# Kernel tuning notes

Hardware: AMD Instinct MI355X
Metric: run time of the kernel (lower is better)

## Reference

```python
import jax, jax.numpy as jnp
import numpy as np

N_NODES = 2000
NEG_SLOPE = 0.01  # torch nn.LeakyReLU default


def setup_inputs() -> dict:
    key = jax.random.key(0)
    ks = jax.random.split(key, 7)
    B, T, N, F, E = 4, 12, N_NODES, 64, 32000
    state = jax.random.normal(ks[0], (B, T, N, F), dtype=jnp.float32)
    feature = jax.random.normal(ks[1], (N, F), dtype=jnp.float32)
    W = jax.random.normal(ks[2], (F, 2 * F), dtype=jnp.float32) / np.sqrt(2 * F)
    b = jnp.zeros((F,), dtype=jnp.float32)
    src = jax.random.randint(ks[3], (E,), 0, N)
    dst = jax.random.randint(ks[4], (E,), 0, N)
    dist = jax.random.uniform(ks[5], (E, 1), dtype=jnp.float32)
    return {"state": state, "feature": feature, "W": W, "b": b,
            "src": src, "dst": dst, "dist": dist}


def reference(state, feature, W, b, src, dst, dist):
    # state: [B,T,N,F] -> node-major [N,B,T,F] (matches unsqueeze/transpose/squeeze)
    s = jnp.moveaxis(state, 2, 0)                       # [N,B,T,F]
    s_src = s[src]                                      # [E,B,T,F] gather
    s_dst = s[dst]                                      # [E,B,T,F]
    h = jnp.concatenate([s_src, s_dst], axis=-1)        # [E,B,T,2F]
    alpha = jnp.einsum('ebtk,fk->ebtf', h, W) + b       # linear 2F->F
    alpha = jnp.where(alpha >= 0, alpha, NEG_SLOPE * alpha)  # LeakyReLU
    alpha = alpha * dist[:, None, None, :]              # dist [E,1] broadcast
    # segment softmax over incoming edges per destination node
    n = s.shape[0]
    m = jax.ops.segment_max(alpha, dst, num_segments=n)        # [N,B,T,F]
    ex = jnp.exp(alpha - m[dst])
    denom = jax.ops.segment_sum(ex, dst, num_segments=n)       # [N,B,T,F]
    w = ex / denom[dst]                                         # [E,B,T,F]
    new_state = jax.ops.segment_sum(w * s_src, dst, num_segments=n)
    new_state = jax.nn.relu(new_state)                  # [N,B,T,F]
    return jnp.moveaxis(new_state, 0, 2)                # [B,T,N,F]
```

## Files before the change

kernel.cpp:

```cpp
#include <hip/hip_runtime.h>
#include <hip/hip_bf16.h>
#include <hip/hip_fp16.h>
#include <math.h>


#define F_DIM 64
#define LOG2E 1.442695040888963f
#define CPAD 128
#define RSTRIDE 128

typedef _Float16 f16x8 __attribute__((ext_vector_type(8)));
typedef float f32x4 __attribute__((ext_vector_type(4)));

__global__ __launch_bounds__(256) void gemm_hist(
    const float* __restrict__ state, const float* __restrict__ W,
    const float* __restrict__ bias,
    unsigned* __restrict__ PSh, __half* __restrict__ P2Bh,
    const int* __restrict__ dst, int* __restrict__ chunk_hist,
    int E, int N, int HB) {
    __shared__ int h[2048];
    int tid = threadIdx.x;
    if ((int)blockIdx.x < HB) {
        int c = blockIdx.x;
        for (int i = tid; i < N; i += 256) h[i] = 0;
        __syncthreads();
        int e = c * 256 + tid;
        if (e < E) atomicAdd(&h[dst[e]], 1);
        __syncthreads();
        for (int d = tid; d < N; d += 256)
            chunk_hist[d * CPAD + c] = h[d];
        return;
    }
    int gb = blockIdx.x - HB;
    int wv = tid >> 6, lane = tid & 63;
    int l15 = lane & 15, l4 = lane >> 4;

    f16x8 bf[8][2];
#pragma unroll
    for (int ct = 0; ct < 8; ++ct) {
        int j = ct * 16 + l15;
        const float* wp = (j < 64) ? (W + j * 128) : (W + (j - 64) * 128 + 64);
#pragma unroll
        for (int kh = 0; kh < 2; ++kh) {
            const float* p = wp + kh * 32 + l4 * 8;
            float4 w0 = *(const float4*)p;
            float4 w1 = *(const float4*)(p + 4);
            f16x8 hh;
            hh[0] = (_Float16)w0.x; hh[1] = (_Float16)w0.y;
            hh[2] = (_Float16)w0.z; hh[3] = (_Float16)w0.w;
            hh[4] = (_Float16)w1.x; hh[5] = (_Float16)w1.y;
            hh[6] = (_Float16)w1.z; hh[7] = (_Float16)w1.w;
            bf[ct][kh] = hh;
        }
    }
    float b0 = bias[l15], b1 = bias[16 + l15], b2 = bias[32 + l15], b3 = bias[48 + l15];

    int r = gb * 64 + wv * 16;

    const float* ap = state + (long)(r + l15) * 64 + l4 * 8;
    float4 a0 = *(const float4*)ap;
    float4 a1 = *(const float4*)(ap + 4);
    float4 a2 = *(const float4*)(ap + 32);
    float4 a3 = *(const float4*)(ap + 36);
    f16x8 af0, af1;
    af0[0] = (_Float16)a0.x; af0[1] = (_Float16)a0.y;
    af0[2] = (_Float16)a0.z; af0[3] = (_Float16)a0.w;
    af0[4] = (_Float16)a1.x; af0[5] = (_Float16)a1.y;
    af0[6] = (_Float16)a1.z; af0[7] = (_Float16)a1.w;
    af1[0] = (_Float16)a2.x; af1[1] = (_Float16)a2.y;
    af1[2] = (_Float16)a2.z; af1[3] = (_Float16)a2.w;
    af1[4] = (_Float16)a3.x; af1[5] = (_Float16)a3.y;
    af1[6] = (_Float16)a3.z; af1[7] = (_Float16)a3.w;

    f32x4 zero = {0.f, 0.f, 0.f, 0.f};
    f32x4 acc[8];
#pragma unroll
    for (int ct = 0; ct < 8; ++ct) {
        acc[ct] = __builtin_amdgcn_mfma_f32_16x16x32_f16(af0, bf[ct][0], zero, 0, 0, 0);
        acc[ct] = __builtin_amdgcn_mfma_f32_16x16x32_f16(af1, bf[ct][1], acc[ct], 0, 0, 0);
    }

    float bb0[4] = {b0, b1, b2, b3};
#pragma unroll
    for (int reg = 0; reg < 4; ++reg) {
        long rr = r + l4 * 4 + reg;
        const float* sp = state + rr * 64;
#pragma unroll
        for (int ct = 0; ct < 4; ++ct) {
            float sval = sp[ct * 16 + l15];
            __half2 hh = __floats2half2_rn(acc[ct][reg], sval);
            PSh[rr * 64 + ct * 16 + l15] = *(unsigned*)&hh;
        }
#pragma unroll
        for (int ct = 4; ct < 8; ++ct) {
            P2Bh[rr * 64 + (ct - 4) * 16 + l15] =
                __float2half(acc[ct][reg] + bb0[ct - 4]);
        }
    }
}

__global__ void binscan_kernel(int* __restrict__ chunk_hist, int* __restrict__ counts,
                               int* __restrict__ esrc, float* __restrict__ edist,
                               int N, int C) {
    int wave = (blockIdx.x * blockDim.x + threadIdx.x) >> 6;
    int lane = threadIdx.x & 63;
    if (wave >= N) return;
    int* row = chunk_hist + wave * CPAD;
    int i0 = 2 * lane, i1 = 2 * lane + 1;
    int v0 = (i0 < C) ? row[i0] : 0;
    int v1 = (i1 < C) ? row[i1] : 0;
    int s = v0 + v1;
    int acc = s;
#pragma unroll
    for (int d = 1; d < 64; d <<= 1) {
        int up = __shfl_up(acc, d);
        if (lane >= d) acc += up;
    }
    int excl = acc - s;
    if (i0 < C) row[i0] = excl;
    if (i1 < C) row[i1] = excl + v0;
    int total = __shfl(acc, 63);
    if (lane == 63) counts[wave] = total;
    int* er = esrc + wave * RSTRIDE;
    float* dr = edist + wave * RSTRIDE;
    if (i0 >= total) { er[i0] = 0; dr[i0] = 0.f; }
    if (i1 >= total) { er[i1] = 0; dr[i1] = 0.f; }
}

__global__ void scatter2_kernel(const int* __restrict__ dst, const int* __restrict__ src,
                                const float* __restrict__ dist,
                                const int* __restrict__ chunk_hist,
                                int* __restrict__ esrc, float* __restrict__ edist, int E) {
    __shared__ int sdst[256];
    int t = threadIdx.x, c = blockIdx.x;
    int e = c * 256 + t;
    int d = (e < E) ? dst[e] : -1;
    sdst[t] = d;
    __syncthreads();
    if (e >= E) return;
    int cnt = 0;
#pragma unroll 8
    for (int j = 0; j < 256; j++)
        cnt += (j < t && sdst[j] == d) ? 1 : 0;
    int off = chunk_hist[d * CPAD + c] + cnt;
    if (off < RSTRIDE) {
        esrc[d * RSTRIDE + off] = src[e] << 8;
        edist[d * RSTRIDE + off] = dist[e] * LOG2E;
    }
}


#define ECOMP(U, D, P2V, DEN, NUM)                                        \
    {                                                                     \
        float x;                                                          \
        asm("v_fma_mix_f32 %0, %1, %2, %3 op_sel:[0,0,0] op_sel_hi:[1,0,0]" \
            : "=v"(x) : "v"(U), "v"(fone), "v"(P2V));                     \
        float y0 = x * (D);                                               \
        float y1 = 0.01f * y0;                                            \
        float y = fmaxf(y0, y1);                                          \
        float p = __builtin_amdgcn_exp2f(y);                              \
        DEN += p;                                                         \
        asm("v_fma_mix_f32 %0, %1, %2, %0 op_sel:[0,1,0] op_sel_hi:[0,1,0]" \
            : "+v"(NUM) : "v"(p), "v"(U));                                \
    }

#define G4E4(EP, DP, Q, P2V, D0, D1, M0, M1)                              \
    {                                                                     \
        int4   sq = (EP)[Q];                                              \
        float4 dq = (DP)[Q];                                              \
        unsigned q0 = *(const unsigned*)(PSb + sq.x + f4);                \
        unsigned q1 = *(const unsigned*)(PSb + sq.y + f4);                \
        unsigned q2 = *(const unsigned*)(PSb + sq.z + f4);                \
        unsigned q3 = *(const unsigned*)(PSb + sq.w + f4);                \
        ECOMP(q0, dq.x, P2V, D0, M0)                                      \
        ECOMP(q1, dq.y, P2V, D1, M1)                                      \
        ECOMP(q2, dq.z, P2V, D0, M0)                                      \
        ECOMP(q3, dq.w, P2V, D1, M1)                                      \
    }

__global__ __launch_bounds__(64, 8) void gat_kernel(
    const unsigned* __restrict__ PSh, const __half* __restrict__ P2Bh,
    const int* __restrict__ esrc, const float* __restrict__ edist,
    const int* __restrict__ counts,
    float* __restrict__ out, int N, int NBT) {
    int b = blockIdx.x;
    int xcd = b & 7, j = b >> 3;
    int pr = j / 6, sub = j % 6;
    int f = threadIdx.x & 63;
    int bt = xcd * 6 + sub;
    const char* PSb = (const char*)PSh + (size_t)bt * N * 256;
    int f4 = f << 2;
    int n0 = pr * 2;
    int cnt0 = counts[n0], cnt1 = counts[n0 + 1];
    const int4*   ep0 = (const int4*)(esrc + n0 * RSTRIDE);
    const float4* dp0 = (const float4*)(edist + n0 * RSTRIDE);
    const int4*   ep1 = ep0 + (RSTRIDE / 4);
    const float4* dp1 = dp0 + (RSTRIDE / 4);
    int ob0 = ((bt * N + n0) << 6) + f;
    float p2_0 = __half2float(P2Bh[ob0]);
    float p2_1 = __half2float(P2Bh[ob0 + 64]);
    unsigned z = *(const unsigned*)(PSb + f4);
    float zs = __half22float2(*(const __half2*)&z).y;
    float fone = 1.0f;
    int cm0 = (cnt0 > RSTRIDE) ? RSTRIDE : cnt0;
    int cm1 = (cnt1 > RSTRIDE) ? RSTRIDE : cnt1;
    int nq0 = (cm0 + 3) >> 2, nq1 = (cm1 + 3) >> 2;
    int nqmin = (nq0 < nq1) ? nq0 : nq1;
    float denA0 = 0.f, denA1 = 0.f, numA0 = 0.f, numA1 = 0.f;
    float denB0 = 0.f, denB1 = 0.f, numB0 = 0.f, numB1 = 0.f;
    for (int q = 0; q < nqmin; ++q) {
        int4   sa = ep0[q], sb = ep1[q];
        float4 da = dp0[q], db = dp1[q];
        unsigned a0 = *(const unsigned*)(PSb + sa.x + f4);
        unsigned b0 = *(const unsigned*)(PSb + sb.x + f4);
        unsigned a1 = *(const unsigned*)(PSb + sa.y + f4);
        unsigned b1 = *(const unsigned*)(PSb + sb.y + f4);
        unsigned a2 = *(const unsigned*)(PSb + sa.z + f4);
        unsigned b2 = *(const unsigned*)(PSb + sb.z + f4);
        unsigned a3 = *(const unsigned*)(PSb + sa.w + f4);
        unsigned b3 = *(const unsigned*)(PSb + sb.w + f4);
        ECOMP(a0, da.x, p2_0, denA0, numA0)
        ECOMP(b0, db.x, p2_1, denB0, numB0)
        ECOMP(a1, da.y, p2_0, denA1, numA1)
        ECOMP(b1, db.y, p2_1, denB1, numB1)
        ECOMP(a2, da.z, p2_0, denA0, numA0)
        ECOMP(b2, db.z, p2_1, denB0, numB0)
        ECOMP(a3, da.w, p2_0, denA1, numA1)
        ECOMP(b3, db.w, p2_1, denB1, numB1)
    }
    for (int q = nqmin; q < nq0; ++q)
        G4E4(ep0, dp0, q, p2_0, denA0, denA1, numA0, numA1)
    for (int q = nqmin; q < nq1; ++q)
        G4E4(ep1, dp1, q, p2_1, denB0, denB1, numB0, numB1)
    float npad0 = (float)((nq0 << 2) - cm0);
    float npad1 = (float)((nq1 << 2) - cm1);
    float o0 = (cnt0 > 0)
        ? fmaxf((numA0 + numA1 - npad0 * zs) / (denA0 + denA1 - npad0), 0.f) : 0.f;
    float o1 = (cnt1 > 0)
        ? fmaxf((numB0 + numB1 - npad1 * zs) / (denB0 + denB1 - npad1), 0.f) : 0.f;
    out[ob0] = o0;
    out[ob0 + 64] = o1;
}


extern "C" void kernel_launch(void* const* d_in, const int* in_sizes, int n_in,
                              void* d_out, int out_size, void* d_ws, size_t ws_size,
                              hipStream_t stream) {
    const float* state = (const float*)d_in[0];
    const float* W     = (const float*)d_in[2];
    const float* bias  = (const float*)d_in[3];
    const int*   src   = (const int*)d_in[4];
    const int*   dst   = (const int*)d_in[5];
    const float* dist  = (const float*)d_in[6];
    float* out = (float*)d_out;

    int N   = in_sizes[1] / F_DIM;
    int E   = in_sizes[4];
    int NBT = in_sizes[0] / (N * F_DIM);
    int C   = (E + 255) / 256;

    size_t pelems = (size_t)NBT * N * F_DIM;
    unsigned* PSh = (unsigned*)d_ws;
    __half* P2Bh = (__half*)(PSh + pelems);
    int* counts     = (int*)(P2Bh + pelems);
    int* chunk_hist = counts + 2048;
    int* esrc       = chunk_hist + N * CPAD;
    float* edist    = (float*)(esrc + N * RSTRIDE);

    int total_rows = NBT * N;
    gemm_hist<<<C + total_rows / 64, 256, 0, stream>>>(state, W, bias, PSh, P2Bh,
                                                       dst, chunk_hist, E, N, C);
    binscan_kernel<<<(N * 64 + 255) / 256, 256, 0, stream>>>(chunk_hist, counts,
                                                             esrc, edist, N, C);
    scatter2_kernel<<<C, 256, 0, stream>>>(dst, src, dist, chunk_hist, esrc, edist, E);

    gat_kernel<<<8 * 6 * (N / 2), 64, 0, stream>>>(PSh, P2Bh, esrc, edist, counts,
                                                   out, N, NBT);
}
```

Before: 79.91 us.

## Merge bin scan into scatter kernel using transposed chunk histogram

The chunk histogram is stored transposed (chunk-major), and the separate scan kernel is removed. Each scatter thread now sums the prefix over earlier chunks for its destination itself, and extra blocks compute per-node totals and zero-pad the edge lists. This drops one kernel launch and its dependency barrier, at the cost of redundant prefix reads: up to 125 strided loads per edge thread.

```diff
diff --git a/kernel.cpp b/kernel.cpp
--- a/kernel.cpp
+++ b/kernel.cpp
@@ -6,7 +6,7 @@
 
 #define F_DIM 64
 #define LOG2E 1.442695040888963f
-#define CPAD 128
+#define DSTR 2048
 #define RSTRIDE 128
 
 typedef _Float16 f16x8 __attribute__((ext_vector_type(8)));
@@ -16,7 +16,7 @@
     const float* __restrict__ state, const float* __restrict__ W,
     const float* __restrict__ bias,
     unsigned* __restrict__ PSh, __half* __restrict__ P2Bh,
-    const int* __restrict__ dst, int* __restrict__ chunk_hist,
+    const int* __restrict__ dst, int* __restrict__ chunk_hist_T,
     int E, int N, int HB) {
     __shared__ int h[2048];
     int tid = threadIdx.x;
@@ -28,7 +28,7 @@
         if (e < E) atomicAdd(&h[dst[e]], 1);
         __syncthreads();
         for (int d = tid; d < N; d += 256)
-            chunk_hist[d * CPAD + c] = h[d];
+            chunk_hist_T[c * DSTR + d] = h[d];
         return;
     }
     int gb = blockIdx.x - HB;
@@ -99,53 +99,51 @@
     }
 }
 
-__global__ void binscan_kernel(int* __restrict__ chunk_hist, int* __restrict__ counts,
-                               int* __restrict__ esrc, float* __restrict__ edist,
-                               int N, int C) {
-    int wave = (blockIdx.x * blockDim.x + threadIdx.x) >> 6;
-    int lane = threadIdx.x & 63;
-    if (wave >= N) return;
-    int* row = chunk_hist + wave * CPAD;
-    int i0 = 2 * lane, i1 = 2 * lane + 1;
-    int v0 = (i0 < C) ? row[i0] : 0;
-    int v1 = (i1 < C) ? row[i1] : 0;
-    int s = v0 + v1;
-    int acc = s;
-#pragma unroll
-    for (int d = 1; d < 64; d <<= 1) {
-        int up = __shfl_up(acc, d);
-        if (lane >= d) acc += up;
-    }
-    int excl = acc - s;
-    if (i0 < C) row[i0] = excl;
-    if (i1 < C) row[i1] = excl + v0;
-    int total = __shfl(acc, 63);
-    if (lane == 63) counts[wave] = total;
-    int* er = esrc + wave * RSTRIDE;
-    float* dr = edist + wave * RSTRIDE;
-    if (i0 >= total) { er[i0] = 0; dr[i0] = 0.f; }
-    if (i1 >= total) { er[i1] = 0; dr[i1] = 0.f; }
-}
-
-__global__ void scatter2_kernel(const int* __restrict__ dst, const int* __restrict__ src,
-                                const float* __restrict__ dist,
-                                const int* __restrict__ chunk_hist,
-                                int* __restrict__ esrc, float* __restrict__ edist, int E) {
-    __shared__ int sdst[256];
-    int t = threadIdx.x, c = blockIdx.x;
-    int e = c * 256 + t;
-    int d = (e < E) ? dst[e] : -1;
-    sdst[t] = d;
-    __syncthreads();
-    if (e >= E) return;
-    int cnt = 0;
+__global__ void scatter_pad_kernel(const int* __restrict__ dst, const int* __restrict__ src,
+                                   const float* __restrict__ dist,
+                                   const int* __restrict__ chunk_hist_T,
+                                   int* __restrict__ counts,
+                                   int* __restrict__ esrc, float* __restrict__ edist,
+                                   int E, int N, int C) {
+    int c = blockIdx.x;
+    int t = threadIdx.x;
+    if (c < C) {
+        __shared__ int sdst[256];
+        int e = c * 256 + t;
+        int d = (e < E) ? dst[e] : -1;
+        sdst[t] = d;
+        __syncthreads();
+        if (e >= E) return;
+        int rk = 0;
 #pragma unroll 8
-    for (int j = 0; j < 256; j++)
-        cnt += (j < t && sdst[j] == d) ? 1 : 0;
-    int off = chunk_hist[d * CPAD + c] + cnt;
-    if (off < RSTRIDE) {
-        esrc[d * RSTRIDE + off] = src[e] << 8;
-        edist[d * RSTRIDE + off] = dist[e] * LOG2E;
+        for (int j = 0; j < 256; j++)
+            rk += (j < t && sdst[j] == d) ? 1 : 0;
+        int pre = 0;
+        int c2 = 0;
+        for (; c2 + 4 <= c; c2 += 4) {
+            int p0 = chunk_hist_T[(c2 + 0) * DSTR + d];
+            int p1 = chunk_hist_T[(c2 + 1) * DSTR + d];
+            int p2 = chunk_hist_T[(c2 + 2) * DSTR + d];
+            int p3 = chunk_hist_T[(c2 + 3) * DSTR + d];
+            pre += p0 + p1 + p2 + p3;
+        }
+        for (; c2 < c; ++c2) pre += chunk_hist_T[c2 * DSTR + d];
+        int off = pre + rk;
+        if (off < RSTRIDE) {
+            esrc[d * RSTRIDE + off] = src[e] << 8;
+            edist[d * RSTRIDE + off] = dist[e] * LOG2E;
+        }
+    } else {
+        int d = (c - C) * 256 + t;
+        if (d >= N) return;
+        int tot = 0;
+        for (int c2 = 0; c2 < C; ++c2)
+            tot += chunk_hist_T[c2 * DSTR + d];
+        counts[d] = tot;
+        int st = (tot < RSTRIDE) ? tot : RSTRIDE;
+        int* er = esrc + d * RSTRIDE;
+        float* dr = edist + d * RSTRIDE;
+        for (int i = st; i < RSTRIDE; ++i) { er[i] = 0; dr[i] = 0.f; }
     }
 }
 
@@ -262,17 +260,16 @@
     size_t pelems = (size_t)NBT * N * F_DIM;
     unsigned* PSh = (unsigned*)d_ws;
     __half* P2Bh = (__half*)(PSh + pelems);
-    int* counts     = (int*)(P2Bh + pelems);
-    int* chunk_hist = counts + 2048;
-    int* esrc       = chunk_hist + N * CPAD;
-    float* edist    = (float*)(esrc + N * RSTRIDE);
+    int* counts       = (int*)(P2Bh + pelems);
+    int* chunk_hist_T = counts + 2048;
+    int* esrc         = chunk_hist_T + 128 * DSTR;
+    float* edist      = (float*)(esrc + 2048 * RSTRIDE);
 
     int total_rows = NBT * N;
     gemm_hist<<<C + total_rows / 64, 256, 0, stream>>>(state, W, bias, PSh, P2Bh,
-                                                       dst, chunk_hist, E, N, C);
-    binscan_kernel<<<(N * 64 + 255) / 256, 256, 0, stream>>>(chunk_hist, counts,
-                                                             esrc, edist, N, C);
-    scatter2_kernel<<<C, 256, 0, stream>>>(dst, src, dist, chunk_hist, esrc, edist, E);
+                                                       dst, chunk_hist_T, E, N, C);
+    scatter_pad_kernel<<<C + (N + 255) / 256, 256, 0, stream>>>(
+        dst, src, dist, chunk_hist_T, counts, esrc, edist, E, N, C);
 
     gat_kernel<<<8 * 6 * (N / 2), 64, 0, stream>>>(PSh, P2Bh, esrc, edist, counts,
                                                    out, N, NBT);
```

Measured after the change: 97.32 us. 21.8% more time.
